# Optimization experiments

Measured on AMD Instinct MI355X. Metric: run time of the kernel, lower is better.

The kernel has to match this reference:

```python
import jax, jax.numpy as jnp
import numpy as np

ALPHA = 0.5
TEMP = 0.1
TEMP2 = 0.05  # hardcoded in nt_xent_loss2
NUM_CLASSES = 10
EPS = 1e-12


def setup_inputs() -> dict:
    key = jax.random.key(0)
    k1, k2, k3 = jax.random.split(key, 3)
    B, D, C = 4096, 256, NUM_CLASSES
    cls_feats = jax.random.normal(k1, (B, D), dtype=jnp.float32)
    predicts = jax.random.normal(k2, (B, C), dtype=jnp.float32)
    targets = jax.random.randint(k3, (B,), 0, C)
    return {"cls_feats": cls_feats, "predicts": predicts, "targets": targets}


def _nt_xent_loss(feats, labels):
    B = feats.shape[0]
    eye = jnp.eye(B, dtype=bool)
    same = labels[:, None] == labels[None, :]
    mask = (same & ~eye).astype(feats.dtype)            # positives, no diagonal
    s = jnp.einsum('bd,cd->bc', feats, feats) / TEMP     # [B,B]
    s = jnp.where(eye, 0.0, s)                           # subtract diag_embed(diag)
    logits = s - jax.lax.stop_gradient(jnp.max(s, axis=1, keepdims=True))
    log_denom = jnp.log(jnp.sum(jnp.exp(logits), axis=1, keepdims=True) + EPS)
    log_prob = logits * mask - log_denom
    mask_sum = jnp.sum(mask, axis=1)
    mask_sum = jnp.where(mask_sum == 0, 1.0, mask_sum)
    pos_logits = jnp.sum(mask * log_prob, axis=1) / mask_sum
    return -jnp.mean(pos_logits)


def _nt_xent_loss2(feats, labels):
    B = feats.shape[0]
    eye = jnp.eye(B, dtype=bool)
    same = labels[:, None] == labels[None, :]
    mask = (same & ~eye).astype(feats.dtype)
    diff = ~same                                         # mask2 / different-label pairs
    S = (feats @ feats.T) / TEMP2                        # [B,B]
    val = jnp.where(diff, S, 0.0)                        # dot * different_label_mask

    # The torch loop body depends only on labels[i] -> compute once per class.
    def per_class(c):
        neg = labels != c                                # negatives of class c
        in_sub = neg[:, None] & neg[None, :]             # submatrix membership
        # row max over columns restricted to the negative set
        maxdot = jnp.max(jnp.where(neg[None, :], val, -jnp.inf), axis=1)  # [B]
        shifted = jnp.where(in_sub, val - maxdot[:, None], -jnp.inf)
        s_c = jnp.sum(jnp.exp(shifted))                  # exp_terms.sum()
        n_c = jnp.sum(jnp.where(in_sub, diff, False).astype(jnp.float32))
        return s_c, n_c

    sums, counts = jax.lax.map(jax.checkpoint(per_class), jnp.arange(NUM_CLASSES))
    x = sums[labels]                                     # [B] negtive_dot_negtive_sum
    negsum = counts[labels]                              # [B]
    all_zero = jnp.all(negsum == 0)
    x = jnp.where(all_zero, x, x / negsum)
    log_prob_row = -jnp.log(x + EPS)                     # constant across each row
    mask_sum = jnp.sum(mask, axis=1)
    mask_sum_safe = jnp.where(mask_sum == 0, 1.0, mask_sum)
    pos_logits = (mask_sum * log_prob_row) / mask_sum_safe
    return -jnp.mean(pos_logits)


def reference(cls_feats, predicts, targets):
    norm = jnp.maximum(jnp.linalg.norm(cls_feats, axis=-1, keepdims=True), EPS)
    feats = cls_feats / norm                             # F.normalize(dim=-1)
    logp = jax.nn.log_softmax(predicts, axis=-1)
    ce = -jnp.mean(jnp.take_along_axis(logp, targets[:, None], axis=1)[:, 0])
    cl = _nt_xent_loss(feats, targets)
    tl = _nt_xent_loss2(feats, targets)
    return (1.0 - ALPHA) * ce + ALPHA * cl + 0.5 * ALPHA * tl
```

## Files before the change

### kernel.cpp

```cpp
#include <hip/hip_runtime.h>
#include <math.h>

#define B 4096
#define D 256
#define NC 10
#define LDW 65
#define ZERO4 22528

typedef __attribute__((ext_vector_type(8))) short bf16x8;
typedef __attribute__((ext_vector_type(4))) float f32x4;

__device__ __forceinline__ unsigned short f2bf(float x) {
    unsigned int u = __float_as_uint(x);
    u += 0x7FFFu + ((u >> 16) & 1u);
    return (unsigned short)(u >> 16);
}

__global__ void prep_kernel(const float* __restrict__ feats, const float* __restrict__ pred,
                            const int* __restrict__ tg, unsigned short* __restrict__ fN,
                            float4* __restrict__ bigz, int* __restrict__ h,
                            float* __restrict__ scal) {
    __shared__ int histL[16];
    const int t = threadIdx.x, w = t >> 6, l = t & 63;
    const int gid = t >> 4, lg = t & 15;
    const int r0 = blockIdx.x * 16;
    if (t < 16) histL[t] = 0;
    __syncthreads();
    int zi = blockIdx.x * 256 + t;
    if (zi < ZERO4) bigz[zi] = (float4){0.f, 0.f, 0.f, 0.f};

    int row = r0 + gid;
    float4 v[4];
#pragma unroll
    for (int k = 0; k < 4; k++) v[k] = ((const float4*)feats)[row * 64 + lg * 4 + k];
    float ss = 0.f;
#pragma unroll
    for (int k = 0; k < 4; k++)
        ss += v[k].x * v[k].x + v[k].y * v[k].y + v[k].z * v[k].z + v[k].w * v[k].w;
#pragma unroll
    for (int o = 1; o < 16; o <<= 1) ss += __shfl_xor(ss, o);
    float inv = 1.0f / fmaxf(sqrtf(ss), 1e-12f);
    bf16x8 o0, o1;
#pragma unroll
    for (int k = 0; k < 4; k++) {
        const float* vp = (const float*)&v[k];
        if (k < 2) {
#pragma unroll
            for (int e = 0; e < 4; e++) o0[k * 4 + e] = (short)f2bf(vp[e] * inv);
        } else {
#pragma unroll
            for (int e = 0; e < 4; e++) o1[(k - 2) * 4 + e] = (short)f2bf(vp[e] * inv);
        }
    }
    ((bf16x8*)fN)[row * 32 + lg * 2 + 0] = o0;
    ((bf16x8*)fN)[row * 32 + lg * 2 + 1] = o1;

    if (w == 0 && l < 16) atomicAdd(&histL[tg[r0 + l]], 1);
    if (w == 1 && l < 16) {
        const float* p = pred + (r0 + l) * NC;
        float m = p[0];
#pragma unroll
        for (int c = 1; c < NC; c++) m = fmaxf(m, p[c]);
        float s = 0.f;
#pragma unroll
        for (int c = 0; c < NC; c++) s += __expf(p[c] - m);
        float vce = m + logf(s) - p[tg[r0 + l]];
#pragma unroll
        for (int o = 1; o < 16; o <<= 1) vce += __shfl_xor(vce, o);
        if (l == 0) atomicAdd(&scal[0], vce);
    }
    __syncthreads();
    if (t < NC && histL[t]) atomicAdd(&h[t], histL[t]);
}

__global__ void scatter_kernel(const int* __restrict__ tg, const int* __restrict__ h,
                               int* __restrict__ ccnt, int* __restrict__ labelP,
                               int* __restrict__ origIdx, int* __restrict__ posOf) {
    __shared__ int cb[16];
    __shared__ int wcnt[4][16];
    __shared__ int wabs[4][16];
    const int t = threadIdx.x, w = t >> 6, l = t & 63;
    const int row = blockIdx.x * 256 + t;
    const int c = tg[row];
    if (t == 0) {
        int s = 0;
        for (int cc = 0; cc < NC; cc++) { cb[cc] = s; s += h[cc]; }
    }
    unsigned long long below = (l == 0) ? 0ull : ((~0ull) >> (64 - l));
    int rank = 0;
#pragma unroll
    for (int cc = 0; cc < NC; cc++) {
        unsigned long long m = __ballot(c == cc);
        if (c == cc) rank = __popcll(m & below);
        if (l == 0) wcnt[w][cc] = __popcll(m);
    }
    __syncthreads();
    if (t < NC) {
        int pre[4], s = 0;
#pragma unroll
        for (int ww = 0; ww < 4; ww++) { pre[ww] = s; s += wcnt[ww][t]; }
        int b = cb[t] + atomicAdd(&ccnt[t], s);
#pragma unroll
        for (int ww = 0; ww < 4; ww++) wabs[ww][t] = b + pre[ww];
    }
    __syncthreads();
    int pos = wabs[w][c] + rank;
    labelP[pos] = c;
    origIdx[pos] = row;
    posOf[row] = pos;
}

__launch_bounds__(256)
__global__ void gemm_kernel(const unsigned short* __restrict__ fN,
                            const int* __restrict__ tg, const int* __restrict__ labelP,
                            const int* __restrict__ origIdx, const int* __restrict__ posOf,
                            float* __restrict__ E1, float* __restrict__ P1,
                            float* __restrict__ E2G, int* __restrict__ M2K) {
    __shared__ float scW[4][16 * LDW];
    __shared__ int labS[256];
    __shared__ float E2L[64 * 11];
    __shared__ int M2L[64 * 11];
    __shared__ float E1L[64], P1L[64];

    const int t = threadIdx.x;
    const int w = t >> 6, l = t & 63;
    const int qr = l >> 4, lm = l & 15;
    const int row0 = blockIdx.x * 64;
    const int colB = blockIdx.y * 256;

    labS[t] = labelP[colB + t];
    for (int s = t; s < 64 * 11; s += 256) { E2L[s] = 0.f; M2L[s] = 0; }
    if (t < 64) { E1L[t] = 0.f; P1L[t] = 0.f; }

    int offB[4];
#pragma unroll
    for (int nb = 0; nb < 4; nb++)
        offB[nb] = origIdx[colB + w * 64 + nb * 16 + lm] * D + qr * 8;

    const unsigned short* pa = fN + (row0 + lm) * D + qr * 8;

    f32x4 acc[4][4];
#pragma unroll
    for (int mb = 0; mb < 4; mb++)
#pragma unroll
        for (int nb = 0; nb < 4; nb++) acc[mb][nb] = (f32x4){0.f, 0.f, 0.f, 0.f};

#pragma unroll 2
    for (int ks = 0; ks < 8; ks++) {
        bf16x8 af[4], bfr[4];
#pragma unroll
        for (int mb = 0; mb < 4; mb++) af[mb] = *(const bf16x8*)(pa + mb * 16 * D + ks * 32);
#pragma unroll
        for (int nb = 0; nb < 4; nb++) bfr[nb] = *(const bf16x8*)(fN + offB[nb] + ks * 32);
#pragma unroll
        for (int mb = 0; mb < 4; mb++)
#pragma unroll
            for (int nb = 0; nb < 4; nb++)
                acc[mb][nb] = __builtin_amdgcn_mfma_f32_16x16x32_bf16(af[mb], bfr[nb],
                                                                      acc[mb][nb], 0, 0, 0);
    }
    __syncthreads();

    int liR[4], posR[4];
#pragma unroll
    for (int mb = 0; mb < 4; mb++) {
        int rg = row0 + mb * 16 + lm;
        liR[mb] = tg[rg];
        posR[mb] = posOf[rg];
    }

#pragma unroll
    for (int mb = 0; mb < 4; mb++) {
#pragma unroll
        for (int nb = 0; nb < 4; nb++)
#pragma unroll
            for (int r = 0; r < 4; r++)
                scW[w][(qr * 4 + r) * LDW + nb * 16 + lm] = acc[mb][nb][r];
        const int rowL = mb * 16 + lm;
        const int li = liR[mb];
        const int posr = posR[mb];
        const float* srow = &scW[w][lm * LDW + qr * 16];
        const int colg0 = colB + w * 64 + qr * 16;
        float e1sum = 0.f, p1sum = 0.f;
        int seg = -1; float segE = 0.f; int segK = 0;
#pragma unroll
        for (int j = 0; j < 16; j++) {
            float g = srow[j];
            int lj = labS[w * 64 + qr * 16 + j];
            bool diag = (colg0 + j == posr);
            bool same = (lj == li);
            float s1 = diag ? 0.f : 10.f * g;
            float e1 = __expf(s1);
            e1sum += e1;
            p1sum += (same && !diag) ? s1 : 0.f;
            if (lj != seg) {
                if (seg >= 0) {
                    if (segE > 0.f) atomicAdd(&E2L[rowL * 11 + seg], segE);
                    if (segK > 0) atomicMax(&M2L[rowL * 11 + seg], segK);
                }
                seg = lj; segE = 0.f; segK = 0;
            }
            if (!same) {
                segE += e1 * e1;
                segK = max(segK, __float_as_int(20.f * g + 64.f));
            }
        }
        if (seg >= 0) {
            if (segE > 0.f) atomicAdd(&E2L[rowL * 11 + seg], segE);
            if (segK > 0) atomicMax(&M2L[rowL * 11 + seg], segK);
        }
        e1sum += __shfl_xor(e1sum, 16); e1sum += __shfl_xor(e1sum, 32);
        p1sum += __shfl_xor(p1sum, 16); p1sum += __shfl_xor(p1sum, 32);
        if (qr == 0) {
            atomicAdd(&E1L[rowL], e1sum);
            atomicAdd(&P1L[rowL], p1sum);
        }
    }
    __syncthreads();

    if (t < 64) {
        atomicAdd(&E1[row0 + t], E1L[t]);
        atomicAdd(&P1[row0 + t], P1L[t]);
    }
    for (int s = t; s < 64 * NC; s += 256) {
        int r = s / NC, c = s - r * NC;
        float e = E2L[r * 11 + c];
        int k = M2L[r * 11 + c];
        if (e > 0.f) atomicAdd(&E2G[(row0 + r) * NC + c], e);
        if (k > 0) atomicMax(&M2K[(row0 + r) * NC + c], k);
    }
}

__global__ void rowfin_kernel(const int* __restrict__ tg, const int* __restrict__ h,
                              const float* __restrict__ E1, const float* __restrict__ P1,
                              const float* __restrict__ E2G, const int* __restrict__ M2K,
                              float* __restrict__ sums, float* __restrict__ scal,
                              int* __restrict__ done, float* __restrict__ out) {
    __shared__ float ssumL[16];
    __shared__ int lastS;
    const int t = threadIdx.x;
    if (t < 16) ssumL[t] = 0.f;
    __syncthreads();
    const int i = blockIdx.x * 64 + t;
    const int li = tg[i];
    float E2[NC], M2[NC];
#pragma unroll
    for (int k = 0; k < NC; k++) {
        E2[k] = E2G[i * NC + k];
        int key = M2K[i * NC + k];
        M2[k] = (key > 0) ? (__int_as_float(key) - 64.f) : -3.0e38f;
    }
    const int hl = h[li];
    E2[li] = (float)hl;
    M2[li] = 0.f;
    float m1 = -3.0e38f, m2 = -3.0e38f;
    int a1 = -1;
#pragma unroll
    for (int k = 0; k < NC; k++) {
        float v = M2[k];
        if (v > m1) { m2 = m1; m1 = v; a1 = k; }
        else if (v > m2) m2 = v;
    }
    float Es = 0.f;
#pragma unroll
    for (int k = 0; k < NC; k++) Es += E2[k];
#pragma unroll
    for (int c = 0; c < NC; c++) {
        if (c == li) continue;
        float T = Es - E2[c];
        if (T > 0.f) {
            float md = (a1 == c) ? m2 : m1;
            atomicAdd(&ssumL[c], __expf(-md) * T);
        }
    }
    float cn = (float)(hl - 1);
    float pos1 = (cn > 0.f) ? (P1[i] / cn - logf(E1[i])) : 0.f;
#pragma unroll
    for (int o = 1; o < 64; o <<= 1) pos1 += __shfl_xor(pos1, o);
    if (t == 0) atomicAdd(&scal[1], pos1);
    __syncthreads();
    if (t < NC && ssumL[t] > 0.f) atomicAdd(&sums[t], ssumL[t]);

    __threadfence();
    if (t == 0) lastS = (atomicAdd(done, 1) == 63);
    __syncthreads();
    if (lastS && t == 0) {
        int hh[NC];
        long long S2 = 0;
        for (int c = 0; c < NC; c++) { hh[c] = h[c]; S2 += (long long)hh[c] * hh[c]; }
        float ncs[NC];
        int az = 1;
        for (int c = 0; c < NC; c++) {
            long long M = (long long)B - hh[c];
            long long n = M * M - (S2 - (long long)hh[c] * hh[c]);
            ncs[c] = (float)n;
            if (hh[c] > 0 && n != 0) az = 0;
        }
        float possum = 0.f;
        for (int c = 0; c < NC; c++) {
            if (hh[c] > 1) {
                float x = atomicAdd(&sums[c], 0.f);
                if (!az) x = x / ncs[c];
                possum += (float)hh[c] * (-logf(x + 1e-12f));
            }
        }
        float ce = scal[0] / (float)B;
        float cl = -(atomicAdd(&scal[1], 0.f) / (float)B);
        float tl = -(possum / (float)B);
        float loss = 0.5f * ce + 0.5f * cl + 0.25f * tl;
        unsigned int bits = __float_as_uint(loss);
        unsigned int hedged = (bits & 0xFFFF0000u) | (bits >> 16);
        *(unsigned int*)out = hedged;
    }
}

extern "C" void kernel_launch(void* const* d_in, const int* in_sizes, int n_in,
                              void* d_out, int out_size, void* d_ws, size_t ws_size,
                              hipStream_t stream) {
    (void)in_sizes; (void)n_in; (void)out_size; (void)ws_size;
    const float* feats = (const float*)d_in[0];
    const float* pred = (const float*)d_in[1];
    const int* tg = (const int*)d_in[2];
    float* out = (float*)d_out;

    unsigned short* fN = (unsigned short*)d_ws;
    float* E1 = (float*)(fN + B * D);
    float* P1 = E1 + B;
    float* E2G = P1 + B;
    int* M2K = (int*)(E2G + B * NC);
    int* h = M2K + B * NC;
    int* ccnt = h + 16;
    float* sums = (float*)(ccnt + 16);
    float* scal = sums + 16;
    int* done = (int*)(scal + 16);
    int* labelP = done + 16;
    int* origIdx = labelP + B;
    int* posOf = origIdx + B;

    hipMemsetAsync(h, 0, 5 * 16 * sizeof(int), stream);

    prep_kernel<<<B / 16, 256, 0, stream>>>(feats, pred, tg, fN, (float4*)E1, h, scal);
    scatter_kernel<<<B / 256, 256, 0, stream>>>(tg, h, ccnt, labelP, origIdx, posOf);
    gemm_kernel<<<dim3(B / 64, B / 256), 256, 0, stream>>>(fN, tg, labelP, origIdx, posOf,
                                                           E1, P1, E2G, M2K);
    rowfin_kernel<<<B / 64, 64, 0, stream>>>(tg, h, E1, P1, E2G, M2K, sums, scal, done, out);
}
```

Baseline: 141.1 us.

## Drop memset, single-block scatter, narrower GEMM tiles with register epilogue

Removes the hipMemsetAsync by zeroing accumulators inside the GEMM kernel and writing per-block partial sums instead of atomics. The histogram moves into a single 1024-thread scatter block, and the CE and pos1 reductions become deterministic partial arrays. The GEMM column tile shrinks from 256 to 128 so there are more blocks, and the epilogue now works directly from MFMA accumulator registers instead of going through an LDS transpose. The risks are a serial single-block scatter, more atomics per element in the epilogue, and less B-fragment reuse per A load.

```diff
diff --git a/kernel.cpp b/kernel.cpp
--- a/kernel.cpp
+++ b/kernel.cpp
@@ -4,7 +4,6 @@
 #define B 4096
 #define D 256
 #define NC 10
-#define LDW 65
 #define ZERO4 22528
 
 typedef __attribute__((ext_vector_type(8))) short bf16x8;
@@ -18,14 +17,10 @@
 
 __global__ void prep_kernel(const float* __restrict__ feats, const float* __restrict__ pred,
                             const int* __restrict__ tg, unsigned short* __restrict__ fN,
-                            float4* __restrict__ bigz, int* __restrict__ h,
-                            float* __restrict__ scal) {
-    __shared__ int histL[16];
+                            float4* __restrict__ bigz, float* __restrict__ ceP) {
     const int t = threadIdx.x, w = t >> 6, l = t & 63;
     const int gid = t >> 4, lg = t & 15;
     const int r0 = blockIdx.x * 16;
-    if (t < 16) histL[t] = 0;
-    __syncthreads();
     int zi = blockIdx.x * 256 + t;
     if (zi < ZERO4) bigz[zi] = (float4){0.f, 0.f, 0.f, 0.f};
 
@@ -55,7 +50,6 @@
     ((bf16x8*)fN)[row * 32 + lg * 2 + 0] = o0;
     ((bf16x8*)fN)[row * 32 + lg * 2 + 1] = o1;
 
-    if (w == 0 && l < 16) atomicAdd(&histL[tg[r0 + l]], 1);
     if (w == 1 && l < 16) {
         const float* p = pred + (r0 + l) * NC;
         float m = p[0];
@@ -67,47 +61,58 @@
         float vce = m + logf(s) - p[tg[r0 + l]];
 #pragma unroll
         for (int o = 1; o < 16; o <<= 1) vce += __shfl_xor(vce, o);
-        if (l == 0) atomicAdd(&scal[0], vce);
-    }
-    __syncthreads();
-    if (t < NC && histL[t]) atomicAdd(&h[t], histL[t]);
-}
-
-__global__ void scatter_kernel(const int* __restrict__ tg, const int* __restrict__ h,
-                               int* __restrict__ ccnt, int* __restrict__ labelP,
-                               int* __restrict__ origIdx, int* __restrict__ posOf) {
-    __shared__ int cb[16];
-    __shared__ int wcnt[4][16];
-    __shared__ int wabs[4][16];
+        if (l == 0) ceP[blockIdx.x] = vce;
+    }
+}
+
+__global__ void scatter_kernel(const int* __restrict__ tg, int* __restrict__ h,
+                               int* __restrict__ labelP, int* __restrict__ origIdx,
+                               int* __restrict__ posOf) {
+    __shared__ int hist[16], runBase[16];
+    __shared__ int wcnt[16][16], wbase[16][16];
     const int t = threadIdx.x, w = t >> 6, l = t & 63;
-    const int row = blockIdx.x * 256 + t;
-    const int c = tg[row];
+    if (t < 16) hist[t] = 0;
+    __syncthreads();
+    int cls[4];
+#pragma unroll
+    for (int ch = 0; ch < 4; ch++) cls[ch] = tg[ch * 1024 + t];
+#pragma unroll
+    for (int ch = 0; ch < 4; ch++)
+#pragma unroll
+        for (int c = 0; c < NC; c++) {
+            unsigned long long m = __ballot(cls[ch] == c);
+            if (l == 0 && m) atomicAdd(&hist[c], __popcll(m));
+        }
+    __syncthreads();
     if (t == 0) {
         int s = 0;
-        for (int cc = 0; cc < NC; cc++) { cb[cc] = s; s += h[cc]; }
-    }
+        for (int c = 0; c < NC; c++) { runBase[c] = s; s += hist[c]; }
+    }
+    if (t < 16) h[t] = hist[t];
+    __syncthreads();
     unsigned long long below = (l == 0) ? 0ull : ((~0ull) >> (64 - l));
-    int rank = 0;
-#pragma unroll
-    for (int cc = 0; cc < NC; cc++) {
-        unsigned long long m = __ballot(c == cc);
-        if (c == cc) rank = __popcll(m & below);
-        if (l == 0) wcnt[w][cc] = __popcll(m);
-    }
-    __syncthreads();
-    if (t < NC) {
-        int pre[4], s = 0;
-#pragma unroll
-        for (int ww = 0; ww < 4; ww++) { pre[ww] = s; s += wcnt[ww][t]; }
-        int b = cb[t] + atomicAdd(&ccnt[t], s);
-#pragma unroll
-        for (int ww = 0; ww < 4; ww++) wabs[ww][t] = b + pre[ww];
-    }
-    __syncthreads();
-    int pos = wabs[w][c] + rank;
-    labelP[pos] = c;
-    origIdx[pos] = row;
-    posOf[row] = pos;
+    for (int ch = 0; ch < 4; ch++) {
+        int c = cls[ch], rank = 0;
+#pragma unroll
+        for (int cc = 0; cc < NC; cc++) {
+            unsigned long long m = __ballot(c == cc);
+            if (c == cc) rank = __popcll(m & below);
+            if (l == 0) wcnt[w][cc] = __popcll(m);
+        }
+        __syncthreads();
+        if (t < NC) {
+            int s = 0;
+#pragma unroll
+            for (int ww = 0; ww < 16; ww++) { wbase[ww][t] = runBase[t] + s; s += wcnt[ww][t]; }
+            runBase[t] += s;
+        }
+        __syncthreads();
+        int pos = wbase[w][c] + rank;
+        int row = ch * 1024 + t;
+        labelP[pos] = c;
+        origIdx[pos] = row;
+        posOf[row] = pos;
+    }
 }
 
 __launch_bounds__(256)
@@ -115,9 +120,10 @@
                             const int* __restrict__ tg, const int* __restrict__ labelP,
                             const int* __restrict__ origIdx, const int* __restrict__ posOf,
                             float* __restrict__ E1, float* __restrict__ P1,
-                            float* __restrict__ E2G, int* __restrict__ M2K) {
-    __shared__ float scW[4][16 * LDW];
-    __shared__ int labS[256];
+                            float* __restrict__ E2G, int* __restrict__ M2K,
+                            float* __restrict__ sums, int* __restrict__ done2) {
+    __shared__ int labS[128];
+    __shared__ int tgS[64], posS[64];
     __shared__ float E2L[64 * 11];
     __shared__ int M2L[64 * 11];
     __shared__ float E1L[64], P1L[64];
@@ -126,96 +132,82 @@
     const int w = t >> 6, l = t & 63;
     const int qr = l >> 4, lm = l & 15;
     const int row0 = blockIdx.x * 64;
-    const int colB = blockIdx.y * 256;
-
-    labS[t] = labelP[colB + t];
+    const int colB = blockIdx.y * 128;
+
+    if (blockIdx.x == 0 && blockIdx.y == 0) {
+        if (t < 16) sums[t] = 0.f;
+        if (t == 0) *done2 = 0;
+    }
+    if (t < 128) labS[t] = labelP[colB + t];
+    if (t < 64) { tgS[t] = tg[row0 + t]; posS[t] = posOf[row0 + t]; E1L[t] = 0.f; P1L[t] = 0.f; }
     for (int s = t; s < 64 * 11; s += 256) { E2L[s] = 0.f; M2L[s] = 0; }
-    if (t < 64) { E1L[t] = 0.f; P1L[t] = 0.f; }
-
-    int offB[4];
-#pragma unroll
-    for (int nb = 0; nb < 4; nb++)
-        offB[nb] = origIdx[colB + w * 64 + nb * 16 + lm] * D + qr * 8;
-
+
+    const int offB0 = origIdx[colB + w * 32 + lm] * D + qr * 8;
+    const int offB1 = origIdx[colB + w * 32 + 16 + lm] * D + qr * 8;
     const unsigned short* pa = fN + (row0 + lm) * D + qr * 8;
 
-    f32x4 acc[4][4];
-#pragma unroll
-    for (int mb = 0; mb < 4; mb++)
-#pragma unroll
-        for (int nb = 0; nb < 4; nb++) acc[mb][nb] = (f32x4){0.f, 0.f, 0.f, 0.f};
+    f32x4 acc[4][2];
+#pragma unroll
+    for (int mb = 0; mb < 4; mb++) {
+        acc[mb][0] = (f32x4){0.f, 0.f, 0.f, 0.f};
+        acc[mb][1] = (f32x4){0.f, 0.f, 0.f, 0.f};
+    }
 
 #pragma unroll 2
     for (int ks = 0; ks < 8; ks++) {
-        bf16x8 af[4], bfr[4];
+        bf16x8 af[4], b0, b1;
 #pragma unroll
         for (int mb = 0; mb < 4; mb++) af[mb] = *(const bf16x8*)(pa + mb * 16 * D + ks * 32);
-#pragma unroll
-        for (int nb = 0; nb < 4; nb++) bfr[nb] = *(const bf16x8*)(fN + offB[nb] + ks * 32);
-#pragma unroll
-        for (int mb = 0; mb < 4; mb++)
-#pragma unroll
-            for (int nb = 0; nb < 4; nb++)
-                acc[mb][nb] = __builtin_amdgcn_mfma_f32_16x16x32_bf16(af[mb], bfr[nb],
-                                                                      acc[mb][nb], 0, 0, 0);
-    }
-    __syncthreads();
-
-    int liR[4], posR[4];
-#pragma unroll
-    for (int mb = 0; mb < 4; mb++) {
-        int rg = row0 + mb * 16 + lm;
-        liR[mb] = tg[rg];
-        posR[mb] = posOf[rg];
-    }
-
-#pragma unroll
-    for (int mb = 0; mb < 4; mb++) {
-#pragma unroll
-        for (int nb = 0; nb < 4; nb++)
-#pragma unroll
-            for (int r = 0; r < 4; r++)
-                scW[w][(qr * 4 + r) * LDW + nb * 16 + lm] = acc[mb][nb][r];
-        const int rowL = mb * 16 + lm;
-        const int li = liR[mb];
-        const int posr = posR[mb];
-        const float* srow = &scW[w][lm * LDW + qr * 16];
-        const int colg0 = colB + w * 64 + qr * 16;
-        float e1sum = 0.f, p1sum = 0.f;
-        int seg = -1; float segE = 0.f; int segK = 0;
-#pragma unroll
-        for (int j = 0; j < 16; j++) {
-            float g = srow[j];
-            int lj = labS[w * 64 + qr * 16 + j];
-            bool diag = (colg0 + j == posr);
-            bool same = (lj == li);
-            float s1 = diag ? 0.f : 10.f * g;
-            float e1 = __expf(s1);
-            e1sum += e1;
-            p1sum += (same && !diag) ? s1 : 0.f;
-            if (lj != seg) {
-                if (seg >= 0) {
-                    if (segE > 0.f) atomicAdd(&E2L[rowL * 11 + seg], segE);
-                    if (segK > 0) atomicMax(&M2L[rowL * 11 + seg], segK);
-                }
-                seg = lj; segE = 0.f; segK = 0;
+        b0 = *(const bf16x8*)(fN + offB0 + ks * 32);
+        b1 = *(const bf16x8*)(fN + offB1 + ks * 32);
+#pragma unroll
+        for (int mb = 0; mb < 4; mb++) {
+            acc[mb][0] = __builtin_amdgcn_mfma_f32_16x16x32_bf16(af[mb], b0, acc[mb][0], 0, 0, 0);
+            acc[mb][1] = __builtin_amdgcn_mfma_f32_16x16x32_bf16(af[mb], b1, acc[mb][1], 0, 0, 0);
+        }
+    }
+    __syncthreads();
+
+    const int lab0 = labS[w * 32 + lm], lab1 = labS[w * 32 + 16 + lm];
+    const int colg0 = colB + w * 32 + lm, colg1 = colg0 + 16;
+#pragma unroll
+    for (int mb = 0; mb < 4; mb++)
+#pragma unroll
+        for (int r = 0; r < 4; r++) {
+            const int rowL = mb * 16 + qr * 4 + r;
+            const int li = tgS[rowL], posr = posS[rowL];
+            float g0 = acc[mb][0][r], g1 = acc[mb][1][r];
+            bool d0 = (colg0 == posr), d1 = (colg1 == posr);
+            bool s0 = (lab0 == li), s1 = (lab1 == li);
+            float t0 = d0 ? 0.f : 10.f * g0;
+            float t1 = d1 ? 0.f : 10.f * g1;
+            float e0 = __expf(t0), e1v = __expf(t1);
+            float es = e0 + e1v;
+            float ps = ((s0 && !d0) ? t0 : 0.f) + ((s1 && !d1) ? t1 : 0.f);
+            float E2a = s0 ? 0.f : e0 * e0;
+            float E2b = s1 ? 0.f : e1v * e1v;
+            int K0 = s0 ? 0 : __float_as_int(fmaf(20.f, g0, 64.f));
+            int K1 = s1 ? 0 : __float_as_int(fmaf(20.f, g1, 64.f));
+            if (lab0 == lab1) {
+                float E = E2a + E2b;
+                int K = max(K0, K1);
+                if (E > 0.f) atomicAdd(&E2L[rowL * 11 + lab0], E);
+                if (K > 0) atomicMax(&M2L[rowL * 11 + lab0], K);
+            } else {
+                if (E2a > 0.f) atomicAdd(&E2L[rowL * 11 + lab0], E2a);
+                if (K0 > 0) atomicMax(&M2L[rowL * 11 + lab0], K0);
+                if (E2b > 0.f) atomicAdd(&E2L[rowL * 11 + lab1], E2b);
+                if (K1 > 0) atomicMax(&M2L[rowL * 11 + lab1], K1);
             }
-            if (!same) {
-                segE += e1 * e1;
-                segK = max(segK, __float_as_int(20.f * g + 64.f));
+            es += __shfl_xor(es, 1); ps += __shfl_xor(ps, 1);
+            es += __shfl_xor(es, 2); ps += __shfl_xor(ps, 2);
+            es += __shfl_xor(es, 4); ps += __shfl_xor(ps, 4);
+            es += __shfl_xor(es, 8); ps += __shfl_xor(ps, 8);
+            if (lm == 0) {
+                atomicAdd(&E1L[rowL], es);
+                atomicAdd(&P1L[rowL], ps);
             }
         }
-        if (seg >= 0) {
-            if (segE > 0.f) atomicAdd(&E2L[rowL * 11 + seg], segE);
-            if (segK > 0) atomicMax(&M2L[rowL * 11 + seg], segK);
-        }
-        e1sum += __shfl_xor(e1sum, 16); e1sum += __shfl_xor(e1sum, 32);
-        p1sum += __shfl_xor(p1sum, 16); p1sum += __shfl_xor(p1sum, 32);
-        if (qr == 0) {
-            atomicAdd(&E1L[rowL], e1sum);
-            atomicAdd(&P1L[rowL], p1sum);
-        }
-    }
     __syncthreads();
 
     if (t < 64) {
@@ -234,14 +226,17 @@
 __global__ void rowfin_kernel(const int* __restrict__ tg, const int* __restrict__ h,
                               const float* __restrict__ E1, const float* __restrict__ P1,
                               const float* __restrict__ E2G, const int* __restrict__ M2K,
-                              float* __restrict__ sums, float* __restrict__ scal,
-                              int* __restrict__ done, float* __restrict__ out) {
+                              float* __restrict__ sums, const float* __restrict__ ceP,
+                              float* __restrict__ pos1P, int* __restrict__ done2,
+                              float* __restrict__ out) {
     __shared__ float ssumL[16];
+    __shared__ float wred[4];
+    __shared__ float fin[256];
     __shared__ int lastS;
-    const int t = threadIdx.x;
+    const int t = threadIdx.x, w = t >> 6, l = t & 63;
     if (t < 16) ssumL[t] = 0.f;
     __syncthreads();
-    const int i = blockIdx.x * 64 + t;
+    const int i = blockIdx.x * 256 + t;
     const int li = tg[i];
     float E2[NC], M2[NC];
 #pragma unroll
@@ -277,40 +272,50 @@
     float pos1 = (cn > 0.f) ? (P1[i] / cn - logf(E1[i])) : 0.f;
 #pragma unroll
     for (int o = 1; o < 64; o <<= 1) pos1 += __shfl_xor(pos1, o);
-    if (t == 0) atomicAdd(&scal[1], pos1);
+    if (l == 0) wred[w] = pos1;
     __syncthreads();
     if (t < NC && ssumL[t] > 0.f) atomicAdd(&sums[t], ssumL[t]);
-
+    if (t == 0) pos1P[blockIdx.x] = wred[0] + wred[1] + wred[2] + wred[3];
     __threadfence();
-    if (t == 0) lastS = (atomicAdd(done, 1) == 63);
-    __syncthreads();
-    if (lastS && t == 0) {
-        int hh[NC];
-        long long S2 = 0;
-        for (int c = 0; c < NC; c++) { hh[c] = h[c]; S2 += (long long)hh[c] * hh[c]; }
-        float ncs[NC];
-        int az = 1;
-        for (int c = 0; c < NC; c++) {
-            long long M = (long long)B - hh[c];
-            long long n = M * M - (S2 - (long long)hh[c] * hh[c]);
-            ncs[c] = (float)n;
-            if (hh[c] > 0 && n != 0) az = 0;
-        }
-        float possum = 0.f;
-        for (int c = 0; c < NC; c++) {
-            if (hh[c] > 1) {
-                float x = atomicAdd(&sums[c], 0.f);
-                if (!az) x = x / ncs[c];
-                possum += (float)hh[c] * (-logf(x + 1e-12f));
+    if (t == 0) lastS = (atomicAdd(done2, 1) == 15);
+    __syncthreads();
+    if (lastS) {
+        fin[t] = ceP[t];
+        __syncthreads();
+        for (int o = 128; o > 0; o >>= 1) {
+            if (t < o) fin[t] += fin[t + o];
+            __syncthreads();
+        }
+        if (t == 0) {
+            float p1tot = 0.f;
+            for (int k = 0; k < 16; k++) p1tot += atomicAdd(&pos1P[k], 0.f);
+            int hh[NC];
+            long long S2 = 0;
+            for (int c = 0; c < NC; c++) { hh[c] = h[c]; S2 += (long long)hh[c] * hh[c]; }
+            float ncs[NC];
+            int az = 1;
+            for (int c = 0; c < NC; c++) {
+                long long M = (long long)B - hh[c];
+                long long n = M * M - (S2 - (long long)hh[c] * hh[c]);
+                ncs[c] = (float)n;
+                if (hh[c] > 0 && n != 0) az = 0;
             }
-        }
-        float ce = scal[0] / (float)B;
-        float cl = -(atomicAdd(&scal[1], 0.f) / (float)B);
-        float tl = -(possum / (float)B);
-        float loss = 0.5f * ce + 0.5f * cl + 0.25f * tl;
-        unsigned int bits = __float_as_uint(loss);
-        unsigned int hedged = (bits & 0xFFFF0000u) | (bits >> 16);
-        *(unsigned int*)out = hedged;
+            float possum = 0.f;
+            for (int c = 0; c < NC; c++) {
+                if (hh[c] > 1) {
+                    float x = atomicAdd(&sums[c], 0.f);
+                    if (!az) x = x / ncs[c];
+                    possum += (float)hh[c] * (-logf(x + 1e-12f));
+                }
+            }
+            float ce = fin[0] / (float)B;
+            float cl = -(p1tot / (float)B);
+            float tl = -(possum / (float)B);
+            float loss = 0.5f * ce + 0.5f * cl + 0.25f * tl;
+            unsigned int bits = __float_as_uint(loss);
+            unsigned int hedged = (bits & 0xFFFF0000u) | (bits >> 16);
+            *(unsigned int*)out = hedged;
+        }
     }
 }
 
@@ -329,19 +334,18 @@
     float* E2G = P1 + B;
     int* M2K = (int*)(E2G + B * NC);
     int* h = M2K + B * NC;
-    int* ccnt = h + 16;
-    float* sums = (float*)(ccnt + 16);
-    float* scal = sums + 16;
-    int* done = (int*)(scal + 16);
-    int* labelP = done + 16;
+    float* sums = (float*)(h + 16);
+    int* done2 = (int*)(sums + 16);
+    float* ceP = (float*)(done2 + 16);
+    float* pos1P = ceP + 256;
+    int* labelP = (int*)(pos1P + 16);
     int* origIdx = labelP + B;
     int* posOf = origIdx + B;
 
-    hipMemsetAsync(h, 0, 5 * 16 * sizeof(int), stream);
-
-    prep_kernel<<<B / 16, 256, 0, stream>>>(feats, pred, tg, fN, (float4*)E1, h, scal);
-    scatter_kernel<<<B / 256, 256, 0, stream>>>(tg, h, ccnt, labelP, origIdx, posOf);
-    gemm_kernel<<<dim3(B / 64, B / 256), 256, 0, stream>>>(fN, tg, labelP, origIdx, posOf,
-                                                           E1, P1, E2G, M2K);
-    rowfin_kernel<<<B / 64, 64, 0, stream>>>(tg, h, E1, P1, E2G, M2K, sums, scal, done, out);
-}
+    prep_kernel<<<B / 16, 256, 0, stream>>>(feats, pred, tg, fN, (float4*)E1, ceP);
+    scatter_kernel<<<1, 1024, 0, stream>>>(tg, h, labelP, origIdx, posOf);
+    gemm_kernel<<<dim3(B / 64, B / 128), 256, 0, stream>>>(fN, tg, labelP, origIdx, posOf,
+                                                           E1, P1, E2G, M2K, sums, done2);
+    rowfin_kernel<<<16, 256, 0, stream>>>(tg, h, E1, P1, E2G, M2K, sums, ceP, pos1P,
+                                          done2, out);
+}
```

Measured after the change: 211.3 us. 49.8% more time.
